# Optimization experiments

Measured on AMD Instinct MI355X. Metric: run time of the kernel, lower is better.

Reference implementation:

```python
import jax, jax.numpy as jnp
import numpy as np

# ---- P4M (D4) group: 8 elements, idx = 4*m + r (m: mirror bit, r: rot90 count) ----
G = 8

def _mr(i):
    return i // 4, i % 4

def _gidx(m, r):
    return 4 * (m % 2) + (r % 4)

def _comp(a, b):
    m1, r1 = _mr(a); m2, r2 = _mr(b)
    return _gidx(m1 + m2, (r1 if m2 == 0 else -r1) + r2)

_INV = [next(b for b in range(G) if _comp(a, b) == 0) for a in range(G)]
# _PERM[h, g] = index of h^{-1} * g  (left regular action on the group axis)
_PERM = np.array([[_comp(_INV[h], g) for g in range(G)] for h in range(G)])


def _spatial_transform(K, h):
    # act on the last two (spatial) kernel axes by group element h = mirror^m rot^r
    m, r = _mr(h)
    if m:
        K = jnp.flip(K, axis=-1)
    return jnp.rot90(K, k=r, axes=(-2, -1))


def _transformed_kernels(W):
    # W: [N_out, N_in, G, k, k] -> [G, N_out, N_in, G, k, k], one kernel per output group element
    return jnp.stack([_spatial_transform(W[:, :, _PERM[h]], h) for h in range(G)])


def conv_gg(x, W, padding):
    # group->group convolution. x: [B, N_in, G, H, W]; W: [N_out, N_in, G, k, k]
    B, Ni, _, H, Wd = x.shape
    No, k = W.shape[0], W.shape[-1]
    K = _transformed_kernels(W).reshape(G * No, Ni * G, k, k)
    y = jax.lax.conv_general_dilated(
        x.reshape(B, Ni * G, H, Wd), K, window_strides=(1, 1),
        padding=[(padding, padding), (padding, padding)],
        dimension_numbers=('NCHW', 'OIHW', 'NCHW'))
    Ho, Wo = y.shape[-2], y.shape[-1]
    return y.reshape(B, G, No, Ho, Wo).transpose(0, 2, 1, 3, 4)  # [B, N_out, G, Ho, Wo]


def channel_att_gg(x, W1, W2):
    # squeeze-excite over (channel, group) with group-equivariant weight sharing
    s = x.mean(axis=(-2, -1))                                  # [B, C, G]
    P1 = W1[:, :, _PERM]                                       # [M, C, G_out, G_in]
    t = jax.nn.relu(jnp.einsum('mcog,bcg->bmo', P1, s))        # [B, M, G]
    P2 = W2[:, :, _PERM]                                       # [C, M, G_out, G_in]
    return jax.nn.sigmoid(jnp.einsum('cmog,bmg->bco', P2, t))  # [B, C, G]


def spatial_att_gg(x, Wsp):
    # CBAM-style: mean/max over channels, group-equivariant 7x7 conv, sigmoid
    p = jnp.stack([x.mean(axis=1), x.max(axis=1)], axis=1)     # [B, 2, G, H, W]
    return jax.nn.sigmoid(conv_gg(p, Wsp, padding=Wsp.shape[-1] // 2))  # [B, 1, G, H, W]


def f_att_conv_gg(x, W, Wc1, Wc2, Wsp, padding):
    a_ch = channel_att_gg(x, Wc1, Wc2)[:, :, :, None, None]
    a_sp = spatial_att_gg(x, Wsp)
    return conv_gg(x * a_ch * a_sp, W, padding)


def bn3d(x, gamma, beta, eps=2e-5):
    # training-mode BatchNorm3d: stats over (B, G, H, W) per channel, biased variance
    mu = x.mean(axis=(0, 2, 3, 4), keepdims=True)
    var = ((x - mu) ** 2).mean(axis=(0, 2, 3, 4), keepdims=True)
    return (x - mu) * jax.lax.rsqrt(var + eps) * gamma[None, :, None, None, None] \
        + beta[None, :, None, None, None]


C, MID, K, SPK, B, H = 96, 48, 3, 7, 4, 56  # MID = C // ratio-reduction (ratio = C//2)


def setup_inputs() -> dict:
    key = jax.random.key(0)
    ks = jax.random.split(key, 12)
    def rn(k, shape, scale):
        return jax.random.normal(k, shape, dtype=jnp.float32) * scale
    wsc = float(np.sqrt(2.0 / (C * G * K * K)))
    asc = float(np.sqrt(2.0 / (C * G)))
    ssc = float(np.sqrt(2.0 / (2 * G * SPK * SPK)))
    return {
        'x': rn(ks[0], (B, C, G, H, H), 1.0),
        'bn1_gamma': jnp.ones((C,), jnp.float32), 'bn1_beta': jnp.zeros((C,), jnp.float32),
        'bn2_gamma': jnp.ones((C,), jnp.float32), 'bn2_beta': jnp.zeros((C,), jnp.float32),
        'c1_W': rn(ks[1], (C, C, G, K, K), wsc),
        'c1_att1': rn(ks[2], (MID, C, G), asc), 'c1_att2': rn(ks[3], (C, MID, G), asc),
        'c1_sp': rn(ks[4], (1, 2, G, SPK, SPK), ssc),
        'c2_W': rn(ks[5], (C, C, G, K, K), wsc),
        'c2_att1': rn(ks[6], (MID, C, G), asc), 'c2_att2': rn(ks[7], (C, MID, G), asc),
        'c2_sp': rn(ks[8], (1, 2, G, SPK, SPK), ssc),
    }


def reference(x, bn1_gamma, bn1_beta, bn2_gamma, bn2_beta,
              c1_W, c1_att1, c1_att2, c1_sp,
              c2_W, c2_att1, c2_att2, c2_sp):
    # fiber_map='id', stride=1 -> no group pooling, identity shortcut
    h = f_att_conv_gg(jax.nn.relu(bn3d(x, bn1_gamma, bn1_beta)),
                      c1_W, c1_att1, c1_att2, c1_sp, padding=1)
    h = f_att_conv_gg(jax.nn.relu(bn3d(h, bn2_gamma, bn2_beta)),
                      c2_W, c2_att1, c2_att2, c2_sp, padding=1)
    return x + h
```

## Files before the change

kernel.cpp:

```cpp
#include <hip/hip_runtime.h>
#include <math.h>

#define NG 8
#define C96 96
#define NMID 48
#define HW 56
#define PIX 3136
#define GHW 25088
#define CIN 768
#define NPIXT 9633792
#define BN_N 100352
#define PADW 58
#define PADPIX 3364
#define WTK 589824
#define PPL 3968

typedef __attribute__((ext_vector_type(8))) short bf16x8;
typedef __attribute__((ext_vector_type(4))) float f32x4;

__device__ __forceinline__ int d_comp(int a, int b){
  int m1=a>>2, r1=a&3, m2=b>>2, r2=b&3;
  int m=(m1+m2)&1;
  int r = (m2==0) ? (r1+r2) : (r2-r1);
  r = (r+4)&3;
  return 4*m+r;
}
__device__ __forceinline__ int d_inv(int a){ return (a>>2) ? a : ((4-(a&3))&3); }
__device__ __forceinline__ int d_perm(int h, int g){ return d_comp(d_inv(h), g); }

__device__ __forceinline__ void d_src(int h, int dy, int dx, int n, int* sy, int* sx){
  int r=h&3, m=h>>2, e=n-1;
  int y,x;
  if(r==0){y=dy; x=dx;}
  else if(r==1){y=dx; x=e-dy;}
  else if(r==2){y=e-dy; x=e-dx;}
  else {y=e-dx; x=dy;}
  if(m) x = e-x;
  *sy=y; *sx=x;
}

__device__ __forceinline__ unsigned short f2bf(float f){
  unsigned int u = __builtin_bit_cast(unsigned int, f);
  unsigned int r = (u + 0x7FFFu + ((u>>16)&1u)) >> 16;
  return (unsigned short)r;
}

__device__ __forceinline__ void gload_lds16(const void* g, void* l){
  __builtin_amdgcn_global_load_lds((const __attribute__((address_space(1))) unsigned int*)g,
                                   (__attribute__((address_space(3))) unsigned int*)l, 16, 0, 0);
}

#define VMCNT2() do { asm volatile("s_waitcnt vmcnt(2)" ::: "memory"); \
                      __builtin_amdgcn_sched_barrier(0); } while(0)
#define VMCNT0() do { asm volatile("s_waitcnt vmcnt(0)" ::: "memory"); \
                      __builtin_amdgcn_sched_barrier(0); } while(0)
#define BAR() do { __builtin_amdgcn_s_barrier(); __builtin_amdgcn_sched_barrier(0); } while(0)

__global__ void k_bn_stats(const float* __restrict__ in, float* __restrict__ spart){
  __shared__ float sm[8];
  int c = blockIdx.x, s = blockIdx.y;
  int b = s>>1, half = s&1;
  const float4* p = (const float4*)(in + ((size_t)(b*C96 + c))*GHW) + half*(GHW/8);
  float sum=0.f, sum2=0.f;
  for (int i=threadIdx.x; i<GHW/8; i+=256){
    float4 v = p[i];
    sum  += v.x+v.y+v.z+v.w;
    sum2 += v.x*v.x+v.y*v.y+v.z*v.z+v.w*v.w;
  }
  #pragma unroll
  for (int off=32; off>0; off>>=1){ sum += __shfl_down(sum,off); sum2 += __shfl_down(sum2,off); }
  int lane=threadIdx.x&63, wid=threadIdx.x>>6;
  if(lane==0){ sm[wid]=sum; sm[4+wid]=sum2; }
  __syncthreads();
  if(threadIdx.x==0){
    float a=sm[0]+sm[1]+sm[2]+sm[3], b2=sm[4]+sm[5]+sm[6]+sm[7];
    spart[(c*8+s)*2]   = a;
    spart[(c*8+s)*2+1] = b2;
  }
}

__global__ __launch_bounds__(256) void k_pool(const float* __restrict__ in,
    const float* __restrict__ spart, const float* __restrict__ gamma, const float* __restrict__ beta,
    float* __restrict__ pp){
  __shared__ float scs[C96], shs[C96];
  int tid = threadIdx.x;
  if (tid < C96){
    float s=0.f, s2=0.f;
    #pragma unroll
    for (int k=0;k<8;k++){ s += spart[(tid*8+k)*2]; s2 += spart[(tid*8+k)*2+1]; }
    float mean = s*(1.f/BN_N);
    float var  = s2*(1.f/BN_N) - mean*mean;
    float sc = gamma[tid]*rsqrtf(var + 2e-5f);
    scs[tid] = sc; shs[tid] = beta[tid] - mean*sc;
  }
  __syncthreads();
  int bg = blockIdx.y; int b = bg>>3, g = bg&7;
  int px = blockIdx.x*256 + tid;
  if (px >= PIX) return;
  float pm = 0.f, pmx = 0.f;
  for (int c = 0; c < C96; c++){
    size_t idx = ((size_t)((b*C96 + c)*8 + g))*PIX + px;
    float v = fmaxf(fmaf(in[idx], scs[c], shs[c]), 0.f);
    pm += v; pmx = fmaxf(pmx, v);
  }
  int y = px/HW, x = px - y*HW;
  pp[(size_t)(b*16 + g)*PPL     + (y+3)*64 + (x+3)] = pm;
  pp[(size_t)(b*16 + 8 + g)*PPL + (y+3)*64 + (x+3)] = pmx;
}

__global__ void k_chan(const float* __restrict__ in, const float* __restrict__ spart,
    const float* __restrict__ gamma, const float* __restrict__ beta, float* __restrict__ sout){
  int bcg = blockIdx.x;
  int c = (bcg >> 3) % C96;
  float s=0.f, s2=0.f;
  #pragma unroll
  for (int k=0;k<8;k++){ s += spart[(c*8+k)*2]; s2 += spart[(c*8+k)*2+1]; }
  float mean = s*(1.f/BN_N);
  float var  = s2*(1.f/BN_N) - mean*mean;
  float sc = gamma[c]*rsqrtf(var + 2e-5f);
  float sh = beta[c] - mean*sc;
  const float4* p = (const float4*)(in + (size_t)bcg*PIX);
  float acc=0.f;
  for (int i=threadIdx.x; i<PIX/4; i+=64){
    float4 v = p[i];
    acc += fmaxf(fmaf(v.x,sc,sh),0.f) + fmaxf(fmaf(v.y,sc,sh),0.f)
         + fmaxf(fmaf(v.z,sc,sh),0.f) + fmaxf(fmaf(v.w,sc,sh),0.f);
  }
  #pragma unroll
  for(int off=32;off>0;off>>=1) acc += __shfl_down(acc,off);
  if(threadIdx.x==0) sout[bcg] = acc * (1.f/3136.f);
}

__global__ void k_ca(const float* __restrict__ sbuf, const float* __restrict__ W1,
                     const float* __restrict__ W2, float* __restrict__ ach){
  __shared__ float sl[CIN], tl[NMID*8];
  int b = blockIdx.x, tid = threadIdx.x;
  sl[tid] = sbuf[b*CIN + tid];
  __syncthreads();
  int o = tid & 7;
  int pg[8];
  #pragma unroll
  for (int g=0; g<8; g++) pg[g] = d_perm(o, g);
  if (tid < NMID*8){
    int m = tid >> 3;
    float acc = 0.f;
    for (int c=0; c<C96; c++){
      #pragma unroll
      for (int g=0; g<8; g++) acc += W1[(m*C96+c)*8+pg[g]] * sl[c*8+g];
    }
    tl[tid] = fmaxf(acc, 0.f);
  }
  __syncthreads();
  {
    int c = tid >> 3;
    float acc = 0.f;
    for (int m=0; m<NMID; m++){
      #pragma unroll
      for (int g=0; g<8; g++) acc += W2[(c*NMID+m)*8+pg[g]] * tl[(m<<3)+g];
    }
    ach[b*CIN + tid] = 1.f/(1.f+__expf(-acc));
  }
}

__global__ __launch_bounds__(256) void k_sp_conv(const float* __restrict__ pp,
    const float* __restrict__ Wsp, float* __restrict__ aspt){
  __shared__ float wl[2*8*49];
  int bh = blockIdx.y; int b=bh>>3, h=bh&7;
  for(int idx=threadIdx.x; idx<784; idx+=256){
    int i = idx/392; int rem = idx-i*392;
    int g = rem/49; int kk = rem-g*49;
    int dy=kk/7, dx=kk-dy*7;
    int pg = d_perm(h,g);
    int sy,sx; d_src(h,dy,dx,7,&sy,&sx);
    wl[idx] = Wsp[(i*8+pg)*49 + sy*7+sx] * (i==0 ? (1.f/96.f) : 1.f);
  }
  __syncthreads();
  int pix = blockIdx.x*256 + threadIdx.x;
  if(pix>=PIX) return;
  int y=pix/HW, x=pix-y*HW;
  const float* base = pp + (size_t)(b*16)*PPL + y*64 + x;
  float acc=0.f;
  for(int ig=0; ig<16; ig++){
    const float* pb = base + (size_t)ig*PPL;
    const float* wb = wl + ig*49;
    #pragma unroll
    for(int dy=0; dy<7; dy++){
      #pragma unroll
      for(int dx=0; dx<7; dx++)
        acc = fmaf(pb[dy*64+dx], wb[dy*7+dx], acc);
    }
  }
  aspt[((size_t)b*PIX + pix)*8 + h] = 1.f/(1.f+__expf(-acc));
}

__global__ void k_zerob(uint4* __restrict__ xp, uint4* __restrict__ pp){
  uint4 z = (uint4){0u,0u,0u,0u};
  int i = blockIdx.x*256 + threadIdx.x;
  if (blockIdx.x < 248){ pp[i] = z; return; }
  int r = i - 63488;
  if (r >= 87552) return;
  int b = r / 21888;
  int q = r - b*21888;
  int p = q / 96, j = q - p*96;
  int y, x;
  if (p < 58){ y=0; x=p; }
  else if (p < 116){ y=57; x=p-58; }
  else if (p < 172){ y=p-115; x=0; }
  else { y=p-171; x=57; }
  xp[(size_t)(b*PADPIX + y*PADW + x)*96 + j] = z;
}

__global__ __launch_bounds__(256) void k_mod_t(const float* __restrict__ in,
    const float* __restrict__ spart, const float* __restrict__ gamma, const float* __restrict__ beta,
    const float* __restrict__ ach, const float* __restrict__ aspt,
    unsigned int* __restrict__ XpU){
  __shared__ float tile[64][65];
  __shared__ float scs8[8], shs8[8];
  int b = blockIdx.z;
  int cg0 = blockIdx.y*64;
  int pix0 = blockIdx.x*64;
  int tid = threadIdx.x;
  if (tid < 8){
    int c = (cg0>>3) + tid;
    float s=0.f, s2=0.f;
    #pragma unroll
    for (int k=0;k<8;k++){ s += spart[(c*8+k)*2]; s2 += spart[(c*8+k)*2+1]; }
    float mean = s*(1.f/BN_N);
    float var  = s2*(1.f/BN_N) - mean*mean;
    float sc = gamma[c]*rsqrtf(var + 2e-5f);
    scs8[tid] = sc; shs8[tid] = beta[c] - mean*sc;
  }
  __syncthreads();
  int lane = tid & 63, w = tid >> 6;
  for (int r = w; r < 64; r += 4){
    int cg = cg0 + r;
    float a1 = ach[b*CIN + cg];
    float raw = in[(size_t)(b*CIN + cg)*PIX + pix0 + lane];
    float v = fmaxf(fmaf(raw, scs8[r>>3], shs8[r>>3]), 0.f);
    tile[r][lane] = v * a1;
  }
  __syncthreads();
  int half = lane >> 5;
  int cgA = (lane & 31)*2;
  #pragma unroll
  for (int it = 0; it < 8; it++){
    int p = it*8 + w*2 + half;
    int pix = pix0 + p;
    int y = pix/HW, x = pix - y*HW;
    float2 a2 = *(const float2*)(aspt + ((size_t)b*PIX + pix)*8 + (cgA&7));
    float vA = tile[cgA][p]   * a2.x;
    float vB = tile[cgA+1][p] * a2.y;
    unsigned int u = (unsigned int)f2bf(vA) | ((unsigned int)f2bf(vB) << 16);
    XpU[(((size_t)b*PADPIX + (y+1)*PADW + (x+1))*CIN + cg0 + cgA) >> 1] = u;
  }
}

__global__ void k_ktb2(const float* __restrict__ W1src, const float* __restrict__ W2src,
                       unsigned short* __restrict__ Wt1, unsigned short* __restrict__ Wt2){
  const float* W = blockIdx.y ? W2src : W1src;
  unsigned short* Wt = blockIdx.y ? Wt2 : Wt1;
  int idx = blockIdx.x*256 + threadIdx.x;
  int ci = idx % CIN;
  int t2 = idx / CIN;
  int co = t2 % CIN;
  int kk = t2 / CIN;
  int h = co/C96, o = co - h*C96;
  int i = ci >> 3, g = ci & 7;
  int dy = kk/3, dx = kk - dy*3;
  int sy, sx; d_src(h, dy, dx, 3, &sy, &sx);
  float v = W[((o*C96 + i)*8 + d_perm(h,g))*9 + sy*3 + sx];
  Wt[idx] = f2bf(v);
}

__global__ __launch_bounds__(256, 4) void k_convmf(const unsigned short* __restrict__ Xp,
    const unsigned short* __restrict__ Wt, const float* __restrict__ resid,
    float* __restrict__ out){
  __shared__ unsigned short lds[16384];
  char* ldsb = (char*)lds;
  int tid = threadIdx.x, lane = tid & 63, w = tid >> 6;
  int col = lane & 15, kg = lane >> 4;

  int bid = blockIdx.x;
  int wgid = (bid & 7)*84 + (bid >> 3);
  int m = wgid/112; int rem = wgid - m*112;
  int b = rem/28;  int rp = rem - b*28;
  int y0 = rp*2, co0 = m*128;

  int xgo[4], xds[4];
  #pragma unroll
  for (int t = 0; t < 4; t++){
    int slot = t*256 + tid;
    int row = slot >> 8;
    int px  = (slot >> 2) & 63;
    int g   = slot & 3;
    xgo[t] = (b*PADPIX + (y0+row)*PADW + px)*CIN + g*8;
    xds[t] = slot*16;
  }
  int wgo[2], wds[2];
  #pragma unroll
  for (int j = 0; j < 2; j++){
    wgo[j] = (co0 + w*32 + j*16 + (lane>>2))*CIN + (lane&3)*8;
    wds[j] = 16384 + (w*32 + j*16)*64 + lane*16;
  }
  int awo[2];
  #pragma unroll
  for (int mf = 0; mf < 2; mf++)
    awo[mf] = 16384 + (w*32 + mf*16 + col)*64 + kg*16;
  int bb[7];
  #pragma unroll
  for (int nf=0; nf<7; nf++){
    int q2 = nf*16 + col;
    int qyl = (q2 >= 56) ? 1 : 0;
    int qx = q2 - 56*qyl;
    bb[nf] = qyl*4096 + qx*64 + kg*16;
  }

  f32x4 acc[2][7];
  #pragma unroll
  for (int mf=0; mf<2; mf++)
    #pragma unroll
    for (int nf=0; nf<7; nf++)
      acc[mf][nf] = (f32x4){0.f,0.f,0.f,0.f};

  #pragma unroll
  for (int j = 0; j < 2; j++) gload_lds16(Wt + wgo[j], ldsb + wds[j]);
  #pragma unroll
  for (int t = 0; t < 4; t++) gload_lds16(Xp + xgo[t], ldsb + xds[t]);
  VMCNT0();
  BAR();

  int q = 0;
  for (int chunk = 0; chunk < 24; chunk++){
    int ci0 = chunk << 5;
    #pragma unroll
    for (int kk = 0; kk < 9; kk++){
      int s = chunk*9 + kk;
      if (s < 215){
        int kk2 = (kk == 8) ? 0 : kk+1;
        int c2  = (kk == 8) ? chunk+1 : chunk;
        size_t gofs = (size_t)kk2*WTK + (c2 << 5);
        int dofs = (q^1)*8192;
        #pragma unroll
        for (int j = 0; j < 2; j++) gload_lds16(Wt + gofs + wgo[j], ldsb + dofs + wds[j]);
        VMCNT2();
      } else {
        VMCNT0();
      }
      const int wq = q*8192;
      bf16x8 A0 = *(const bf16x8*)(ldsb + awo[0] + wq);
      bf16x8 A1 = *(const bf16x8*)(ldsb + awo[1] + wq);
      const int dyk = kk/3, dxk = kk - dyk*3;
      const int dofs2 = dyk*4096 + dxk*64;
      __builtin_amdgcn_s_setprio(1);
      #pragma unroll
      for (int nf = 0; nf < 7; nf++){
        bf16x8 B = *(const bf16x8*)(ldsb + bb[nf] + dofs2);
        acc[0][nf] = __builtin_amdgcn_mfma_f32_16x16x32_bf16(A0, B, acc[0][nf], 0,0,0);
        acc[1][nf] = __builtin_amdgcn_mfma_f32_16x16x32_bf16(A1, B, acc[1][nf], 0,0,0);
      }
      __builtin_amdgcn_s_setprio(0);
      q ^= 1;
      if (kk == 8 && chunk < 23){
        BAR();
        #pragma unroll
        for (int t = 0; t < 4; t++) gload_lds16(Xp + xgo[t] + ci0 + 32, ldsb + xds[t]);
        VMCNT0();
        BAR();
      }
    }
  }

  #pragma unroll
  for (int mf = 0; mf < 2; mf++){
    int co_b = co0 + w*32 + mf*16;
    int h = co_b/C96;
    int ob = co_b - h*C96 + kg*4;
    #pragma unroll
    for (int nf = 0; nf < 7; nf++){
      int qq = nf*16 + col;
      #pragma unroll
      for (int r = 0; r < 4; r++){
        size_t oi = ((size_t)((b*C96 + ob + r)*8 + h))*PIX + y0*56 + qq;
        float v = acc[mf][nf][r];
        if (resid) v += resid[oi];
        out[oi] = v;
      }
    }
  }
}

static void run_layer(const float* bn_in,
                      const float* a1W, const float* a2W, const float* spW,
                      const float* bng, const float* bnb,
                      const float* resid, float* convout,
                      float* spart, float* sbuf, float* ach, float* ppP, float* aspt,
                      unsigned short* Wt, unsigned short* Xp, hipStream_t stream)
{
  k_bn_stats<<<dim3(C96,8),256,0,stream>>>(bn_in, spart);
  k_pool<<<dim3(13,32),256,0,stream>>>(bn_in, spart, bng, bnb, ppP);
  k_chan<<<4*C96*NG,64,0,stream>>>(bn_in, spart, bng, bnb, sbuf);
  k_ca<<<4,CIN,0,stream>>>(sbuf, a1W, a2W, ach);
  k_sp_conv<<<dim3(13,32),256,0,stream>>>(ppP, spW, aspt);
  k_mod_t<<<dim3(PIX/64, CIN/64, 4),256,0,stream>>>(bn_in, spart, bng, bnb, ach, aspt, (unsigned int*)Xp);
  k_convmf<<<672,256,0,stream>>>(Xp, Wt, resid, convout);
}

extern "C" void kernel_launch(void* const* d_in, const int* in_sizes, int n_in,
                              void* d_out, int out_size, void* d_ws, size_t ws_size,
                              hipStream_t stream) {
  const float* x    = (const float*)d_in[0];
  const float* bn1g = (const float*)d_in[1];
  const float* bn1b = (const float*)d_in[2];
  const float* bn2g = (const float*)d_in[3];
  const float* bn2b = (const float*)d_in[4];
  const float* c1W  = (const float*)d_in[5];
  const float* c1a1 = (const float*)d_in[6];
  const float* c1a2 = (const float*)d_in[7];
  const float* c1sp = (const float*)d_in[8];
  const float* c2W  = (const float*)d_in[9];
  const float* c2a1 = (const float*)d_in[10];
  const float* c2a2 = (const float*)d_in[11];
  const float* c2sp = (const float*)d_in[12];
  float* out = (float*)d_out;
  float* ws  = (float*)d_ws;

  float* bufA = ws;
  unsigned short* Wt1 = (unsigned short*)(bufA + NPIXT);
  unsigned short* Wt2 = Wt1 + 9*CIN*CIN;
  unsigned short* Xp  = Wt2 + 9*CIN*CIN;
  float* spart = (float*)(Xp + (size_t)4*PADPIX*CIN);
  float* sbuf  = spart + 1536;
  float* ach   = sbuf + 4*C96*NG;
  float* ppP   = ach + 4*C96*NG;
  float* aspt  = ppP + 4*16*PPL;

  k_ktb2<<<dim3((9*CIN*CIN)/256, 2),256,0,stream>>>(c1W, c2W, Wt1, Wt2);
  k_zerob<<<590,256,0,stream>>>((uint4*)Xp, (uint4*)ppP);

  run_layer(x, c1a1, c1a2, c1sp, bn1g, bn1b, nullptr, bufA,
            spart, sbuf, ach, ppP, aspt, Wt1, Xp, stream);
  run_layer(bufA, c2a1, c2a2, c2sp, bn2g, bn2b, x, out,
            spart, sbuf, ach, ppP, aspt, Wt2, Xp, stream);
}
```

Measured before the change: 543.0 us.

## Double-buffer input tiles in conv MFMA kernel and XOR-swizzle LDS layout

```diff
diff --git a/kernel.cpp b/kernel.cpp
--- a/kernel.cpp
+++ b/kernel.cpp
@@ -50,6 +50,8 @@
                                    (__attribute__((address_space(3))) unsigned int*)l, 16, 0, 0);
 }
 
+#define VMCNT6() do { asm volatile("s_waitcnt vmcnt(6)" ::: "memory"); \
+                      __builtin_amdgcn_sched_barrier(0); } while(0)
 #define VMCNT2() do { asm volatile("s_waitcnt vmcnt(2)" ::: "memory"); \
                       __builtin_amdgcn_sched_barrier(0); } while(0)
 #define VMCNT0() do { asm volatile("s_waitcnt vmcnt(0)" ::: "memory"); \
@@ -272,10 +274,10 @@
   Wt[idx] = f2bf(v);
 }
 
-__global__ __launch_bounds__(256, 4) void k_convmf(const unsigned short* __restrict__ Xp,
+__global__ __launch_bounds__(256, 3) void k_convmf(const unsigned short* __restrict__ Xp,
     const unsigned short* __restrict__ Wt, const float* __restrict__ resid,
     float* __restrict__ out){
-  __shared__ unsigned short lds[16384];
+  __shared__ unsigned short lds[24576];
   char* ldsb = (char*)lds;
   int tid = threadIdx.x, lane = tid & 63, w = tid >> 6;
   int col = lane & 15, kg = lane >> 4;
@@ -293,26 +295,35 @@
     int row = slot >> 8;
     int px  = (slot >> 2) & 63;
     int g   = slot & 3;
-    xgo[t] = (b*PADPIX + (y0+row)*PADW + px)*CIN + g*8;
+    int sg  = g ^ ((px >> 1) & 3);
+    xgo[t] = (b*PADPIX + (y0+row)*PADW + px)*CIN + sg*8;
     xds[t] = slot*16;
   }
   int wgo[2], wds[2];
   #pragma unroll
   for (int j = 0; j < 2; j++){
-    wgo[j] = (co0 + w*32 + j*16 + (lane>>2))*CIN + (lane&3)*8;
-    wds[j] = 16384 + (w*32 + j*16)*64 + lane*16;
+    int r  = w*32 + j*16 + (lane>>2);
+    int sg = (lane&3) ^ ((lane>>3)&3);
+    wgo[j] = (co0 + r)*CIN + sg*8;
+    wds[j] = 32768 + r*64 + (lane&3)*16;
   }
   int awo[2];
   #pragma unroll
-  for (int mf = 0; mf < 2; mf++)
-    awo[mf] = 16384 + (w*32 + mf*16 + col)*64 + kg*16;
-  int bb[7];
+  for (int mf = 0; mf < 2; mf++){
+    int r = w*32 + mf*16 + col;
+    awo[mf] = 32768 + r*64 + ((kg ^ ((col>>1)&3)) << 4);
+  }
+  int bb[3][7];
   #pragma unroll
   for (int nf=0; nf<7; nf++){
     int q2 = nf*16 + col;
     int qyl = (q2 >= 56) ? 1 : 0;
     int qx = q2 - 56*qyl;
-    bb[nf] = qyl*4096 + qx*64 + kg*16;
+    #pragma unroll
+    for (int dx=0; dx<3; dx++){
+      int px = qx + dx;
+      bb[dx][nf] = qyl*4096 + px*64 + ((kg ^ ((px>>1)&3)) << 4);
+    }
   }
 
   f32x4 acc[2][7];
@@ -330,43 +341,69 @@
   BAR();
 
   int q = 0;
-  for (int chunk = 0; chunk < 24; chunk++){
-    int ci0 = chunk << 5;
+  for (int chunk = 0; chunk < 23; chunk++){
+    const int xb = (chunk & 1) * 16384;
     #pragma unroll
     for (int kk = 0; kk < 9; kk++){
-      int s = chunk*9 + kk;
-      if (s < 215){
+      {
         int kk2 = (kk == 8) ? 0 : kk+1;
         int c2  = (kk == 8) ? chunk+1 : chunk;
         size_t gofs = (size_t)kk2*WTK + (c2 << 5);
         int dofs = (q^1)*8192;
+        gload_lds16(Wt + gofs + wgo[0], ldsb + dofs + wds[0]);
+        gload_lds16(Wt + gofs + wgo[1], ldsb + dofs + wds[1]);
+      }
+      if (kk == 6){
         #pragma unroll
-        for (int j = 0; j < 2; j++) gload_lds16(Wt + gofs + wgo[j], ldsb + dofs + wds[j]);
-        VMCNT2();
-      } else {
-        VMCNT0();
-      }
+        for (int t = 0; t < 4; t++)
+          gload_lds16(Xp + xgo[t] + (chunk+1)*32, ldsb + (xb^16384) + xds[t]);
+      }
+      if (kk == 6 || kk == 7) VMCNT6();
+      else                    VMCNT2();
       const int wq = q*8192;
       bf16x8 A0 = *(const bf16x8*)(ldsb + awo[0] + wq);
       bf16x8 A1 = *(const bf16x8*)(ldsb + awo[1] + wq);
       const int dyk = kk/3, dxk = kk - dyk*3;
-      const int dofs2 = dyk*4096 + dxk*64;
+      const int dofs2 = xb + dyk*4096;
       __builtin_amdgcn_s_setprio(1);
       #pragma unroll
       for (int nf = 0; nf < 7; nf++){
-        bf16x8 B = *(const bf16x8*)(ldsb + bb[nf] + dofs2);
+        bf16x8 B = *(const bf16x8*)(ldsb + bb[dxk][nf] + dofs2);
         acc[0][nf] = __builtin_amdgcn_mfma_f32_16x16x32_bf16(A0, B, acc[0][nf], 0,0,0);
         acc[1][nf] = __builtin_amdgcn_mfma_f32_16x16x32_bf16(A1, B, acc[1][nf], 0,0,0);
       }
       __builtin_amdgcn_s_setprio(0);
       q ^= 1;
-      if (kk == 8 && chunk < 23){
-        BAR();
-        #pragma unroll
-        for (int t = 0; t < 4; t++) gload_lds16(Xp + xgo[t] + ci0 + 32, ldsb + xds[t]);
+    }
+    BAR();
+  }
+  {
+    const int xb = (23 & 1) * 16384;
+    #pragma unroll
+    for (int kk = 0; kk < 9; kk++){
+      if (kk < 8){
+        size_t gofs = (size_t)(kk+1)*WTK + (23 << 5);
+        int dofs = (q^1)*8192;
+        gload_lds16(Wt + gofs + wgo[0], ldsb + dofs + wds[0]);
+        gload_lds16(Wt + gofs + wgo[1], ldsb + dofs + wds[1]);
+        VMCNT2();
+      } else {
         VMCNT0();
-        BAR();
-      }
+      }
+      const int wq = q*8192;
+      bf16x8 A0 = *(const bf16x8*)(ldsb + awo[0] + wq);
+      bf16x8 A1 = *(const bf16x8*)(ldsb + awo[1] + wq);
+      const int dyk = kk/3, dxk = kk - dyk*3;
+      const int dofs2 = xb + dyk*4096;
+      __builtin_amdgcn_s_setprio(1);
+      #pragma unroll
+      for (int nf = 0; nf < 7; nf++){
+        bf16x8 B = *(const bf16x8*)(ldsb + bb[dxk][nf] + dofs2);
+        acc[0][nf] = __builtin_amdgcn_mfma_f32_16x16x32_bf16(A0, B, acc[0][nf], 0,0,0);
+        acc[1][nf] = __builtin_amdgcn_mfma_f32_16x16x32_bf16(A1, B, acc[1][nf], 0,0,0);
+      }
+      __builtin_amdgcn_s_setprio(0);
+      q ^= 1;
     }
   }
 
```

Result: no change. 544.2 us (+0.2%).
